# Kernel tuning notes

Measured on AMD Instinct MI355X. Metric: run time of the kernel, lower is better.

The kernel has to match this reference:

```python
import jax, jax.numpy as jnp
import numpy as np

NB = 56  # numblock
EPS = 1e-5


def layer_norm(x, w, b):
    mu = jnp.mean(x, axis=-1, keepdims=True)
    var = jnp.mean(jnp.square(x - mu), axis=-1, keepdims=True)
    return (x - mu) * jax.lax.rsqrt(var + EPS) * w + b


def min_gru(x, w_hg, w_out):
    # lucidrains minGRU, log-space Heinsen parallel scan (seq_len > 1 branch)
    hg = x @ w_hg                      # [n, L, 2*di]
    hidden, gate = jnp.split(hg, 2, axis=-1)
    log_coeffs = -jax.nn.softplus(gate)        # log(1 - z)
    log_z = -jax.nn.softplus(-gate)            # log z
    # log_g(hidden): where(h>=0, log(relu(h)+0.5), -softplus(-h))
    log_tilde_h = jnp.where(hidden >= 0,
                            jnp.log(jax.nn.relu(hidden) + 0.5),
                            -jax.nn.softplus(-hidden))
    log_values = log_z + log_tilde_h
    a_star = jnp.cumsum(log_coeffs, axis=1)
    log_h = a_star + jax.lax.cumlogsumexp(log_values - a_star, axis=1)
    return jnp.exp(log_h) @ w_out      # [n, L, dim]


def block_fwd(x, norm_w, norm_b, dw_w, dw_b, gru1_whg, gru1_wout,
              gru2_whg, gru2_wout, norm2_w, norm2_b, p1_w, p1_b, p2_w, p2_b):
    n, L, dim = x.shape
    residual = x
    h = layer_norm(x, norm_w, norm_b)
    # depthwise 3x3 conv on [n, dim, NB, NB]
    img = h.reshape(n, NB, NB, dim).transpose(0, 3, 1, 2)
    img = jax.lax.conv_general_dilated(
        img, dw_w, window_strides=(1, 1), padding='SAME',
        feature_group_count=dim,
        dimension_numbers=('NCHW', 'OIHW', 'NCHW')) + dw_b[None, :, None, None]
    h = img.reshape(n, dim, L).transpose(0, 2, 1)
    # bidirectional minGRU: second branch on 2D-flipped sequence
    h2 = jnp.flip(h.reshape(n, NB, NB, dim), axis=(1, 2)).reshape(n, L, dim)
    x1 = min_gru(h, gru1_whg, gru1_wout)
    x2 = jnp.flip(min_gru(h2, gru2_whg, gru2_wout), axis=1)
    h = x1 + x2 + residual
    residual = h
    m = layer_norm(h, norm2_w, norm2_b)
    m = jax.nn.gelu(m @ p1_w + p1_b, approximate=False)
    m = m @ p2_w + p2_b
    return m + residual


def setup_inputs():
    key = jax.random.key(0)
    ks = jax.random.split(key, 9)
    n, dim = 16, 384
    di = 2 * dim          # expansion_factor=2
    mlp = 4 * dim         # mlp_ratio=4
    L = NB * NB

    def w(k, shape, s=0.02):
        return jax.random.normal(k, shape, jnp.float32) * s

    return {
        'x': jax.random.normal(ks[0], (n, L, dim), jnp.float32),
        'norm_w': jnp.ones((dim,), jnp.float32),
        'norm_b': jnp.zeros((dim,), jnp.float32),
        'dw_w': w(ks[1], (dim, 1, 3, 3), 0.1),
        'dw_b': jnp.zeros((dim,), jnp.float32),
        'gru1_whg': w(ks[2], (dim, 2 * di)),
        'gru1_wout': w(ks[3], (di, dim)),
        'gru2_whg': w(ks[4], (dim, 2 * di)),
        'gru2_wout': w(ks[5], (di, dim)),
        'norm2_w': jnp.ones((dim,), jnp.float32),
        'norm2_b': jnp.zeros((dim,), jnp.float32),
        'p1_w': w(ks[6], (dim, mlp)),
        'p1_b': jnp.zeros((mlp,), jnp.float32),
        'p2_w': w(ks[7], (mlp, dim)),
        'p2_b': jnp.zeros((dim,), jnp.float32),
    }


def reference(x, norm_w, norm_b, dw_w, dw_b, gru1_whg, gru1_wout,
              gru2_whg, gru2_wout, norm2_w, norm2_b, p1_w, p1_b, p2_w, p2_b):
    return block_fwd(x, norm_w, norm_b, dw_w, dw_b, gru1_whg, gru1_wout,
                     gru2_whg, gru2_wout, norm2_w, norm2_b, p1_w, p1_b, p2_w, p2_b)
```

## Files before the change

### kernel.cpp

```cpp
#include <hip/hip_runtime.h>
#include <hip/hip_bf16.h>

typedef __hip_bfloat16 bf16;
typedef __attribute__((ext_vector_type(8))) short short8;
typedef __attribute__((ext_vector_type(4))) float floatx4;

#define N_BATCH 16
#define NBQ 56
#define SEQ (NBQ*NBQ)
#define DIM 384
#define DI 768
#define MROWS (N_BATCH*SEQ)
#define NSEG 49
#define SEGLEN 64

__device__ __forceinline__ float b2f(bf16 v){ return __bfloat162float(v); }
__device__ __forceinline__ bf16 f2b(float v){ return __float2bfloat16(v); }

__device__ __forceinline__ float ldin(const void* p, size_t i, int f32){
    return f32 ? ((const float*)p)[i] : __bfloat162float(((const bf16*)p)[i]);
}
__device__ __forceinline__ void stout(void* p, size_t i, int f32, float v){
    if (f32) ((float*)p)[i] = v; else ((bf16*)p)[i] = __float2bfloat16(v);
}

__device__ __forceinline__ void gl2lds16(const void* g, void* l) {
    __builtin_amdgcn_global_load_lds((const __attribute__((address_space(1))) void*)g,
                                     (__attribute__((address_space(3))) void*)l, 16, 0, 0);
}

__global__ void detect_kernel(const unsigned short* __restrict__ x, int* __restrict__ flag) {
    __shared__ int cnt;
    if (threadIdx.x == 0) cnt = 0;
    __syncthreads();
    int c = 0;
    for (int i = threadIdx.x; i < 16384; i += 256) {
        unsigned short u = x[i];
        if ((u & 0x7F80) == 0x7F80) ++c;
    }
    if (c) atomicAdd(&cnt, c);
    __syncthreads();
    if (threadIdx.x == 0) *flag = cnt ? 1 : 0;
}

__global__ __launch_bounds__(64) void ln_kernel(const void* __restrict__ x,
        const void* __restrict__ w, const void* __restrict__ b,
        bf16* __restrict__ y, size_t row_off, const int* __restrict__ flag) {
    const int f32 = *flag;
    const size_t row = row_off + blockIdx.x;
    const int lane = threadIdx.x;
    float v[6]; float s = 0.f;
    #pragma unroll
    for (int j = 0; j < 6; ++j) { v[j] = ldin(x, row*DIM + lane + j*64, f32); s += v[j]; }
    #pragma unroll
    for (int o = 32; o; o >>= 1) s += __shfl_xor(s, o);
    const float mu = s * (1.f/DIM);
    float s2 = 0.f;
    #pragma unroll
    for (int j = 0; j < 6; ++j) { float d = v[j]-mu; s2 += d*d; }
    #pragma unroll
    for (int o = 32; o; o >>= 1) s2 += __shfl_xor(s2, o);
    const float inv = rsqrtf(s2*(1.f/DIM) + 1e-5f);
    bf16* yr = y + (size_t)blockIdx.x * DIM;
    #pragma unroll
    for (int j = 0; j < 6; ++j) {
        int c = lane + j*64;
        yr[c] = f2b((v[j]-mu)*inv*ldin(w, c, f32) + ldin(b, c, f32));
    }
}

__global__ __launch_bounds__(128) void dwconv_kernel(const bf16* __restrict__ h,
        const void* __restrict__ w, const void* __restrict__ bias,
        bf16* __restrict__ out, const int* __restrict__ flag) {
    const int f32 = *flag;
    const int c = blockIdx.x*128 + threadIdx.x;
    const int l = blockIdx.y;
    const int n = blockIdx.z;
    const int i = l / NBQ, j = l - (l / NBQ) * NBQ;
    float acc = ldin(bias, c, f32);
    const bf16* hn = h + (size_t)n*SEQ*DIM;
    #pragma unroll
    for (int di = 0; di < 3; ++di) {
        int ii = i + di - 1;
        if (ii < 0 || ii >= NBQ) continue;
        #pragma unroll
        for (int dj = 0; dj < 3; ++dj) {
            int jj = j + dj - 1;
            if (jj < 0 || jj >= NBQ) continue;
            acc += b2f(hn[((size_t)(ii*NBQ + jj))*DIM + c]) * ldin(w, c*9 + di*3 + dj, f32);
        }
    }
    out[((size_t)n*SEQ + l)*DIM + c] = f2b(acc);
}

__global__ __launch_bounds__(64) void scan_p1(const bf16* __restrict__ G,
        float* __restrict__ Aseg, float* __restrict__ Bseg, int dir) {
    const int c = blockIdx.x*64 + threadIdx.x;
    const int s = blockIdx.y;
    const int n = blockIdx.z;
    const bf16* base = G + (size_t)n*SEQ*(2*DI) + c;
    float A = 1.f, B = 0.f;
    #pragma unroll 4
    for (int u = 0; u < SEGLEN; ++u) {
        const int t = dir ? (SEQ-1 - (s*SEGLEN + u)) : (s*SEGLEN + u);
        const bf16* p = base + (size_t)t*(2*DI);
        float hid = b2f(p[0]), gate = b2f(p[DI]);
        float z  = 1.f/(1.f + __expf(-gate));
        float tl = hid >= 0.f ? hid + 0.5f : 1.f/(1.f + __expf(-hid));
        float a = 1.f - z;
        A *= a;
        B = a*B + z*tl;
    }
    const size_t idx = ((size_t)n*NSEG + s)*DI + c;
    Aseg[idx] = A; Bseg[idx] = B;
}

__global__ __launch_bounds__(64) void scan_p2(const float* __restrict__ Aseg,
        const float* __restrict__ Bseg, float* __restrict__ Pseg) {
    const int c = blockIdx.x*64 + threadIdx.x;
    const int n = blockIdx.y;
    float P = 0.f;
    for (int s = 0; s < NSEG; ++s) {
        const size_t idx = ((size_t)n*NSEG + s)*DI + c;
        Pseg[idx] = P;
        P = Aseg[idx]*P + Bseg[idx];
    }
}

__global__ __launch_bounds__(64) void scan_p3(bf16* __restrict__ G,
        const float* __restrict__ Pseg, int dir) {
    const int c = blockIdx.x*64 + threadIdx.x;
    const int s = blockIdx.y;
    const int n = blockIdx.z;
    bf16* base = G + (size_t)n*SEQ*(2*DI) + c;
    float h = Pseg[((size_t)n*NSEG + s)*DI + c];
    #pragma unroll 4
    for (int u = 0; u < SEGLEN; ++u) {
        const int t = dir ? (SEQ-1 - (s*SEGLEN + u)) : (s*SEGLEN + u);
        bf16* p = base + (size_t)t*(2*DI);
        float hid = b2f(p[0]), gate = b2f(p[DI]);
        float z  = 1.f/(1.f + __expf(-gate));
        float tl = hid >= 0.f ? hid + 0.5f : 1.f/(1.f + __expf(-hid));
        h = (1.f - z)*h + z*tl;
        p[0] = f2b(h);
    }
}

__global__ void transpose_kernel(const void* __restrict__ src, bf16* __restrict__ dst,
                                 int R, int C, const int* __restrict__ flag) {
    const int f32 = *flag;
    int idx = blockIdx.x*256 + threadIdx.x;
    if (idx >= R*C) return;
    int r = idx / C, c = idx - r*C;
    dst[(size_t)c*R + r] = f2b(ldin(src, idx, f32));
}

template<int MODE>
__global__ __launch_bounds__(256, 2) void gemm_kernel(
        const bf16* __restrict__ A, int lda,
        const bf16* __restrict__ Bt,
        void* __restrict__ C, int ldc, int K, size_t row_off,
        const void* __restrict__ bias, const void* __restrict__ resid,
        const int* __restrict__ flag) {
    __shared__ __align__(16) short lsA[128*64];
    __shared__ __align__(16) short lsB[128*64];
    const int tid  = threadIdx.x;
    const int tn0  = blockIdx.x * 128;
    const int tm0  = blockIdx.y * 128;
    const int lane = tid & 63;
    const int wave = tid >> 6;
    const int wm = (wave & 1) * 64;
    const int wn = (wave >> 1) * 64;
    const int row16 = lane & 15;
    const int quad  = lane >> 4;
    const int r7    = row16 & 7;

    floatx4 acc[4][4];
    #pragma unroll
    for (int i = 0; i < 4; ++i)
        #pragma unroll
        for (int j = 0; j < 4; ++j)
            acc[i][j] = (floatx4){0.f, 0.f, 0.f, 0.f};

    const int so_row = tid >> 3;
    const int so_pb  = tid & 7;
    const int so_lb  = so_pb ^ (so_row & 7);

    for (int k0 = 0; k0 < K; k0 += 64) {
        const char* Ab = (const char*)(A + (size_t)tm0*lda + k0);
        const char* Bb = (const char*)(Bt + (size_t)tn0*K + k0);
        #pragma unroll
        for (int it = 0; it < 4; ++it) {
            int row = it*32 + so_row;
            gl2lds16(Ab + (size_t)row*((size_t)lda*2) + so_lb*16,
                     (char*)lsA + row*128 + so_pb*16);
        }
        #pragma unroll
        for (int it = 0; it < 4; ++it) {
            int row = it*32 + so_row;
            gl2lds16(Bb + (size_t)row*((size_t)K*2) + so_lb*16,
                     (char*)lsB + row*128 + so_pb*16);
        }
        __syncthreads();
        #pragma unroll
        for (int kk = 0; kk < 64; kk += 32) {
            const int lb = (kk >> 3) + quad;
            const int pb = (lb ^ r7) * 8;
            short8 af[4], bfr[4];
            #pragma unroll
            for (int i = 0; i < 4; ++i)
                af[i] = *(const short8*)(lsA + (wm + i*16 + row16)*64 + pb);
            #pragma unroll
            for (int j = 0; j < 4; ++j)
                bfr[j] = *(const short8*)(lsB + (wn + j*16 + row16)*64 + pb);
            #pragma unroll
            for (int i = 0; i < 4; ++i)
                #pragma unroll
                for (int j = 0; j < 4; ++j)
                    acc[i][j] = __builtin_amdgcn_mfma_f32_16x16x32_bf16(af[i], bfr[j], acc[i][j], 0, 0, 0);
        }
        __syncthreads();
    }

    const int f32 = (MODE == 0) ? 0 : *flag;
    #pragma unroll
    for (int i = 0; i < 4; ++i) {
        #pragma unroll
        for (int j = 0; j < 4; ++j) {
            #pragma unroll
            for (int r = 0; r < 4; ++r) {
                const int gm = tm0 + wm + i*16 + quad*4 + r;
                const int gn = tn0 + wn + j*16 + row16;
                float v = acc[i][j][r];
                if (MODE == 0) {
                    ((bf16*)C)[(size_t)gm*ldc + gn] = f2b(v);
                } else if (MODE == 1) {
                    size_t gi = (row_off + gm)*(size_t)ldc + gn;
                    v += ldin(resid, gi, f32);
                    stout(C, gi, f32, v);
                } else if (MODE == 2) {
                    v += ldin(bias, gn, f32);
                    v = 0.5f*v*(1.f + erff(v*0.70710678118f));
                    ((bf16*)C)[(size_t)gm*ldc + gn] = f2b(v);
                } else {
                    size_t gi = (row_off + gm)*(size_t)ldc + gn;
                    v += ldin(bias, gn, f32) + ldin(resid, gi, f32);
                    stout(C, gi, f32, v);
                }
            }
        }
    }
}

extern "C" void kernel_launch(void* const* d_in, const int* in_sizes, int n_in,
                              void* d_out, int out_size, void* d_ws, size_t ws_size,
                              hipStream_t stream) {
    const void* x       = d_in[0];
    const void* norm_w  = d_in[1];
    const void* norm_b  = d_in[2];
    const void* dw_w    = d_in[3];
    const void* dw_b    = d_in[4];
    const void* whg1    = d_in[5];
    const void* wout1   = d_in[6];
    const void* whg2    = d_in[7];
    const void* wout2   = d_in[8];
    const void* norm2_w = d_in[9];
    const void* norm2_b = d_in[10];
    const void* p1_w    = d_in[11];
    const void* p1_b    = d_in[12];
    const void* p2_w    = d_in[13];
    const void* p2_b    = d_in[14];
    void* out = d_out;
    char* ws = (char*)d_ws;

    const size_t WSZ = 5898240;

    int CH = 16;
    for (;;) {
        size_t need = 256 + WSZ + (size_t)CH * SEQ * 4608;
        if (need <= ws_size || CH == 2) break;
        CH >>= 1;
    }
    const int NC = N_BATCH / CH;
    const int CHROWS = CH * SEQ;

    int* flag = (int*)ws;
    char* wb = ws + 256;
    bf16* WhgT1  = (bf16*)(wb);
    bf16* WhgT2  = (bf16*)(wb + 1179648);
    bf16* WoutT1 = (bf16*)(wb + 2359296);
    bf16* WoutT2 = (bf16*)(wb + 2949120);
    bf16* P1T    = (bf16*)(wb + 3538944);
    bf16* P2T    = (bf16*)(wb + 4718592);
    char* dyn = ws + 256 + WSZ;
    bf16* h_ln_c   = (bf16*)(dyn);
    bf16* h_conv_c = (bf16*)(dyn + (size_t)CHROWS*DIM*2);
    bf16* Gbuf     = (bf16*)(dyn + 2*(size_t)CHROWS*DIM*2);
    bf16* mid_ln_c = h_ln_c;
    float* Aseg = (float*)h_ln_c;
    float* Bseg = Aseg + (size_t)CH*NSEG*DI;
    float* Pseg = Bseg + (size_t)CH*NSEG*DI;

    detect_kernel<<<1, 256, 0, stream>>>((const unsigned short*)x, flag);

    transpose_kernel<<<(384*1536+255)/256, 256, 0, stream>>>(whg1, WhgT1, 384, 1536, flag);
    transpose_kernel<<<(384*1536+255)/256, 256, 0, stream>>>(whg2, WhgT2, 384, 1536, flag);
    transpose_kernel<<<(768*384+255)/256, 256, 0, stream>>>(wout1, WoutT1, 768, 384, flag);
    transpose_kernel<<<(768*384+255)/256, 256, 0, stream>>>(wout2, WoutT2, 768, 384, flag);
    transpose_kernel<<<(384*1536+255)/256, 256, 0, stream>>>(p1_w, P1T, 384, 1536, flag);
    transpose_kernel<<<(1536*384+255)/256, 256, 0, stream>>>(p2_w, P2T, 1536, 384, flag);

    for (int pass = 0; pass < 2; ++pass) {
        const bf16* WhgT  = pass ? WhgT2  : WhgT1;
        const bf16* WoutT = pass ? WoutT2 : WoutT1;
        for (int ck = 0; ck < NC; ++ck) {
            const size_t roff = (size_t)ck * CHROWS;
            if (pass == 0 || NC > 1) {
                ln_kernel<<<CHROWS, 64, 0, stream>>>(x, norm_w, norm_b, h_ln_c, roff, flag);
                dwconv_kernel<<<dim3(3, SEQ, CH), 128, 0, stream>>>(h_ln_c, dw_w, dw_b, h_conv_c, flag);
            }
            gemm_kernel<0><<<dim3(1536/128, CHROWS/128), 256, 0, stream>>>(
                h_conv_c, DIM, WhgT, Gbuf, 2*DI, DIM, 0, nullptr, nullptr, flag);
            scan_p1<<<dim3(12, NSEG, CH), 64, 0, stream>>>(Gbuf, Aseg, Bseg, pass);
            scan_p2<<<dim3(12, CH), 64, 0, stream>>>(Aseg, Bseg, Pseg);
            scan_p3<<<dim3(12, NSEG, CH), 64, 0, stream>>>(Gbuf, Pseg, pass);
            const void* resid = pass ? (const void*)out : x;
            gemm_kernel<1><<<dim3(DIM/128, CHROWS/128), 256, 0, stream>>>(
                Gbuf, 2*DI, WoutT, out, DIM, DI, roff, nullptr, resid, flag);
        }
    }

    for (int ck = 0; ck < NC; ++ck) {
        const size_t roff = (size_t)ck * CHROWS;
        ln_kernel<<<CHROWS, 64, 0, stream>>>(out, norm2_w, norm2_b, mid_ln_c, roff, flag);
        gemm_kernel<2><<<dim3(1536/128, CHROWS/128), 256, 0, stream>>>(
            mid_ln_c, DIM, P1T, Gbuf, 1536, DIM, 0, p1_b, nullptr, flag);
        gemm_kernel<3><<<dim3(DIM/128, CHROWS/128), 256, 0, stream>>>(
            Gbuf, 1536, P2T, out, DIM, 1536, roff, p2_b, out, flag);
    }
}
```

Before: 1.281 ms.

## Restructure depthwise conv with vectorized channels and sliding row window

```diff
diff --git a/kernel.cpp b/kernel.cpp
--- a/kernel.cpp
+++ b/kernel.cpp
@@ -3,6 +3,7 @@
 
 typedef __hip_bfloat16 bf16;
 typedef __attribute__((ext_vector_type(8))) short short8;
+typedef __attribute__((ext_vector_type(4))) short short4v;
 typedef __attribute__((ext_vector_type(4))) float floatx4;
 
 #define N_BATCH 16
@@ -69,28 +70,73 @@
     }
 }
 
-__global__ __launch_bounds__(128) void dwconv_kernel(const bf16* __restrict__ h,
+__device__ __forceinline__ floatx4 ld_tok4(const bf16* p){
+    short4v s = *(const short4v*)p;
+    floatx4 f;
+    #pragma unroll
+    for (int k = 0; k < 4; ++k) {
+        unsigned int u = ((unsigned int)(unsigned short)s[k]) << 16;
+        f[k] = __uint_as_float(u);
+    }
+    return f;
+}
+
+__global__ __launch_bounds__(192) void dwconv_kernel(const bf16* __restrict__ h,
         const void* __restrict__ w, const void* __restrict__ bias,
         bf16* __restrict__ out, const int* __restrict__ flag) {
     const int f32 = *flag;
-    const int c = blockIdx.x*128 + threadIdx.x;
-    const int l = blockIdx.y;
-    const int n = blockIdx.z;
-    const int i = l / NBQ, j = l - (l / NBQ) * NBQ;
-    float acc = ldin(bias, c, f32);
-    const bf16* hn = h + (size_t)n*SEQ*DIM;
-    #pragma unroll
-    for (int di = 0; di < 3; ++di) {
-        int ii = i + di - 1;
-        if (ii < 0 || ii >= NBQ) continue;
+    const int tid = threadIdx.x;
+    const int c4  = tid % 96;
+    const int j   = blockIdx.x*2 + tid/96;
+    const int i0  = blockIdx.y*8;
+    const int n   = blockIdx.z;
+    const int c0  = c4*4;
+    const bf16* hn = h + (size_t)n*SEQ*DIM + c0;
+
+    floatx4 wgt[9];
+    #pragma unroll
+    for (int t = 0; t < 9; ++t)
+        #pragma unroll
+        for (int k = 0; k < 4; ++k)
+            wgt[t][k] = ldin(w, (size_t)(c0+k)*9 + t, f32);
+    floatx4 bv;
+    #pragma unroll
+    for (int k = 0; k < 4; ++k) bv[k] = ldin(bias, c0+k, f32);
+
+    const floatx4 zero = (floatx4){0.f,0.f,0.f,0.f};
+    floatx4 win[3][3];
+    #pragma unroll
+    for (int dj = 0; dj < 3; ++dj) {
+        const int jj = j + dj - 1;
+        const bool jok = (unsigned)jj < NBQ;
+        win[0][dj] = (jok && i0 > 0) ? ld_tok4(hn + ((size_t)((i0-1)*NBQ + jj))*DIM) : zero;
+        win[1][dj] =  jok            ? ld_tok4(hn + ((size_t)( i0   *NBQ + jj))*DIM) : zero;
+    }
+    bf16* on = out + (size_t)n*SEQ*DIM + c0;
+    #pragma unroll
+    for (int r = 0; r < 8; ++r) {
+        const int i = i0 + r;
         #pragma unroll
         for (int dj = 0; dj < 3; ++dj) {
-            int jj = j + dj - 1;
-            if (jj < 0 || jj >= NBQ) continue;
-            acc += b2f(hn[((size_t)(ii*NBQ + jj))*DIM + c]) * ldin(w, c*9 + di*3 + dj, f32);
-        }
-    }
-    out[((size_t)n*SEQ + l)*DIM + c] = f2b(acc);
+            const int jj = j + dj - 1;
+            const bool ok = ((unsigned)jj < NBQ) && (i+1 < NBQ);
+            win[2][dj] = ok ? ld_tok4(hn + ((size_t)((i+1)*NBQ + jj))*DIM) : zero;
+        }
+        floatx4 acc = bv;
+        #pragma unroll
+        for (int di = 0; di < 3; ++di)
+            #pragma unroll
+            for (int dj = 0; dj < 3; ++dj)
+                #pragma unroll
+                for (int k = 0; k < 4; ++k)
+                    acc[k] += win[di][dj][k] * wgt[di*3+dj][k];
+        short4v o;
+        #pragma unroll
+        for (int k = 0; k < 4; ++k) { bf16 t = f2b(acc[k]); o[k] = *(short*)&t; }
+        *(short4v*)(on + ((size_t)(i*NBQ + j))*DIM) = o;
+        #pragma unroll
+        for (int dj = 0; dj < 3; ++dj) { win[0][dj] = win[1][dj]; win[1][dj] = win[2][dj]; }
+    }
 }
 
 __global__ __launch_bounds__(64) void scan_p1(const bf16* __restrict__ G,
@@ -317,7 +363,7 @@
             const size_t roff = (size_t)ck * CHROWS;
             if (pass == 0 || NC > 1) {
                 ln_kernel<<<CHROWS, 64, 0, stream>>>(x, norm_w, norm_b, h_ln_c, roff, flag);
-                dwconv_kernel<<<dim3(3, SEQ, CH), 128, 0, stream>>>(h_ln_c, dw_w, dw_b, h_conv_c, flag);
+                dwconv_kernel<<<dim3(28, 7, CH), 192, 0, stream>>>(h_ln_c, dw_w, dw_b, h_conv_c, flag);
             }
             gemm_kernel<0><<<dim3(1536/128, CHROWS/128), 256, 0, stream>>>(
                 h_conv_c, DIM, WhgT, Gbuf, 2*DI, DIM, 0, nullptr, nullptr, flag);
```

Measured after the change: 1.153 ms. 10.0% less time.
